# Kernel optimization log

Hardware: AMD Instinct MI355X
Metric: run time of the kernel (lower is better)

## Reference

```python
import jax, jax.numpy as jnp
import numpy as np

N = 100_000   # nodes
E = 1_600_000 # edges (avg degree 16)
IN = 256
OUT = 128
NEG_SLOPE = 0.01  # torch F.leaky_relu default


def setup_inputs() -> dict:
    key = jax.random.key(0)
    k1, k2, k3, k4, k5 = jax.random.split(key, 5)
    h = jax.random.normal(k1, (N, IN), dtype=jnp.float32)
    W = jax.random.normal(k2, (IN, OUT), dtype=jnp.float32) * 0.05  # fc weight (in->out)
    a = jax.random.normal(k3, (2 * OUT,), dtype=jnp.float32) * 0.05  # attn_fc weight, flattened
    src = jax.random.randint(k4, (E,), 0, N, dtype=jnp.int32)
    dst = jax.random.randint(k5, (E,), 0, N, dtype=jnp.int32)
    return {"h": h, "W": W, "a": a, "src": src, "dst": dst, "counter": 3}


def reference(h, W, a, src, dst, counter):
    out_dim = W.shape[1]
    z = h @ W                               # [N, OUT] = fc(h)
    # edge_attention: e = leaky_relu(attn_fc(cat(z[src], z[dst])))
    s = z @ a[:out_dim]                     # [N] src contribution
    t = z @ a[out_dim:]                     # [N] dst contribution
    e = jax.nn.leaky_relu(s[src] + t[dst], NEG_SLOPE)  # [E]
    # segment softmax over incoming edges of each dst node (fixed across iterations)
    m = jax.ops.segment_max(e, dst, num_segments=N)    # [N]
    w = jnp.exp(e - m[dst])                             # [E]
    denom = jax.ops.segment_sum(w, dst, num_segments=N)  # [N]
    alpha = w / denom[dst]                               # [E]
    # nodes with no in-edges keep their previous h (DGL update_all semantics)
    deg = jax.ops.segment_sum(jnp.ones_like(e), dst, num_segments=N)
    has_in = (deg > 0)[:, None]                          # [N,1]
    hcur = z
    for _ in range(int(counter)):
        agg = jax.ops.segment_sum(alpha[:, None] * hcur[src], dst, num_segments=N)  # [N,OUT]
        hcur = jnp.where(has_in, agg, hcur)
    return hcur
```

## Files before the change

### kernel.cpp

```cpp
#include <hip/hip_runtime.h>
#include <math.h>

#define IN_DIM 256
#define OUT_DIM 128
#define BK 1024
#define NBMAX 128

typedef _Float16 f16;
typedef _Float16 f16x2 __attribute__((ext_vector_type(2)));
typedef _Float16 f16x4 __attribute__((ext_vector_type(4)));
typedef _Float16 f16x8 __attribute__((ext_vector_type(8)));
typedef float    f32x4 __attribute__((ext_vector_type(4)));

static inline size_t align256(size_t x){ return (x + 255) & ~size_t(255); }

__global__ void init_kernel(int* __restrict__ gcount, int NB){
  int i = threadIdx.x;
  if (i < NB) gcount[i] = 0;
}

__global__ __launch_bounds__(256) void wprep_kernel(const float* __restrict__ Wm,
    f16* __restrict__ WThi, f16* __restrict__ WTlo){
  int idx = blockIdx.x*256 + threadIdx.x;
  int k = idx >> 7, n = idx & 127;
  float v = Wm[(size_t)k*OUT_DIM + n];
  f16 hi = (f16)v;
  WThi[(size_t)n*IN_DIM + k] = hi;
  WTlo[(size_t)n*IN_DIM + k] = (f16)(v - (float)hi);
}

__global__ __launch_bounds__(256) void gemm_kernel(const float* __restrict__ h,
    const f16* __restrict__ WThi, const f16* __restrict__ WTlo,
    const float* __restrict__ attn_a,
    float* __restrict__ z, f16* __restrict__ zh,
    float* __restrict__ s_arr, float* __restrict__ t_arr, int N){
  __shared__ f16 Ahi[128][40];
  __shared__ f16 Alo[128][40];
  __shared__ f16 Bhi[128][40];
  __shared__ f16 Blo[128][40];

  const int t = threadIdx.x;
  const int l = t & 63;
  const int w = t >> 6;
  const int g = l >> 4;
  const int m15 = l & 15;
  const int row0 = blockIdx.x * 128;

  float as[8], at[8];
  #pragma unroll
  for (int ct=0; ct<8; ct++){
    as[ct] = attn_a[ct*16 + m15];
    at[ct] = attn_a[OUT_DIM + ct*16 + m15];
  }

  f32x4 acc[2][8];
  #pragma unroll
  for (int i=0;i<2;i++)
    #pragma unroll
    for (int j=0;j<8;j++) acc[i][j] = (f32x4){0.f,0.f,0.f,0.f};

  const int ar = t >> 1;
  const int ahalf = (t & 1) << 4;
  for (int k0 = 0; k0 < IN_DIM; k0 += 32){
    {
      int grow = row0 + ar;
      #pragma unroll
      for (int i=0;i<4;i++){
        float4 v = make_float4(0.f,0.f,0.f,0.f);
        if (grow < N) v = *(const float4*)&h[(size_t)grow*IN_DIM + k0 + ahalf + i*4];
        f16 h0=(f16)v.x, h1=(f16)v.y, h2=(f16)v.z, h3=(f16)v.w;
        f16x4 vh = {h0,h1,h2,h3};
        f16x4 vl = {(f16)(v.x-(float)h0),(f16)(v.y-(float)h1),
                    (f16)(v.z-(float)h2),(f16)(v.w-(float)h3)};
        *(f16x4*)&Ahi[ar][ahalf + i*4] = vh;
        *(f16x4*)&Alo[ar][ahalf + i*4] = vl;
      }
      #pragma unroll
      for (int j=0;j<2;j++){
        *(f16x8*)&Bhi[ar][ahalf + j*8] = *(const f16x8*)&WThi[(size_t)ar*IN_DIM + k0 + ahalf + j*8];
        *(f16x8*)&Blo[ar][ahalf + j*8] = *(const f16x8*)&WTlo[(size_t)ar*IN_DIM + k0 + ahalf + j*8];
      }
    }
    __syncthreads();
    f16x8 ah0 = *(const f16x8*)&Ahi[w*32      + m15][g*8];
    f16x8 ah1 = *(const f16x8*)&Ahi[w*32 + 16 + m15][g*8];
    f16x8 al0 = *(const f16x8*)&Alo[w*32      + m15][g*8];
    f16x8 al1 = *(const f16x8*)&Alo[w*32 + 16 + m15][g*8];
    #pragma unroll
    for (int ct=0; ct<8; ct++){
      f16x8 bh = *(const f16x8*)&Bhi[ct*16 + m15][g*8];
      f16x8 bl = *(const f16x8*)&Blo[ct*16 + m15][g*8];
      acc[0][ct] = __builtin_amdgcn_mfma_f32_16x16x32_f16(ah0, bh, acc[0][ct], 0, 0, 0);
      acc[0][ct] = __builtin_amdgcn_mfma_f32_16x16x32_f16(ah0, bl, acc[0][ct], 0, 0, 0);
      acc[0][ct] = __builtin_amdgcn_mfma_f32_16x16x32_f16(al0, bh, acc[0][ct], 0, 0, 0);
      acc[1][ct] = __builtin_amdgcn_mfma_f32_16x16x32_f16(ah1, bh, acc[1][ct], 0, 0, 0);
      acc[1][ct] = __builtin_amdgcn_mfma_f32_16x16x32_f16(ah1, bl, acc[1][ct], 0, 0, 0);
      acc[1][ct] = __builtin_amdgcn_mfma_f32_16x16x32_f16(al1, bh, acc[1][ct], 0, 0, 0);
    }
    __syncthreads();
  }

  #pragma unroll
  for (int rt=0; rt<2; rt++){
    #pragma unroll
    for (int r=0; r<4; r++){
      int grow = row0 + w*32 + rt*16 + g*4 + r;
      float sp = 0.f, tp = 0.f;
      #pragma unroll
      for (int ct=0; ct<8; ct++){
        float v = acc[rt][ct][r];
        if (grow < N){
          z [(size_t)grow*OUT_DIM + ct*16 + m15] = v;
          zh[(size_t)grow*OUT_DIM + ct*16 + m15] = (f16)v;
        }
        sp = fmaf(v, as[ct], sp);
        tp = fmaf(v, at[ct], tp);
      }
      #pragma unroll
      for (int o=1; o<16; o<<=1){ sp += __shfl_xor(sp,o); tp += __shfl_xor(tp,o); }
      if (m15 == 0 && grow < N){ s_arr[grow] = sp; t_arr[grow] = tp; }
    }
  }
}

__global__ __launch_bounds__(256) void count_kernel(const int* __restrict__ dst,
    int* __restrict__ gcount, int E, int NB){
  __shared__ int lh[NBMAX];
  for (int i=threadIdx.x; i<NB; i+=256) lh[i]=0;
  __syncthreads();
  int i = blockIdx.x*blockDim.x + threadIdx.x;
  int stride = gridDim.x*blockDim.x;
  for (; i<E; i+=stride) atomicAdd(&lh[dst[i]>>10], 1);
  __syncthreads();
  for (int i=threadIdx.x; i<NB; i+=256){
    int c = lh[i];
    if (c) atomicAdd(&gcount[i], c);
  }
}

__global__ __launch_bounds__(128) void scanb_kernel(const int* __restrict__ gcount,
    int* __restrict__ gbase, int* __restrict__ gcursor, int* __restrict__ offs,
    int NB, int N, int E){
  int tid = threadIdx.x;
  int v = (tid < NB) ? gcount[tid] : 0;
  int lane = tid & 63, wv = tid >> 6;
  int x = v;
  #pragma unroll
  for (int o=1;o<64;o<<=1){ int y = __shfl_up(x,o); if (lane>=o) x += y; }
  __shared__ int wt[2];
  if (lane==63) wt[wv] = x;
  __syncthreads();
  int off = wv ? wt[0] : 0;
  int excl = off + x - v;
  if (tid < NB){ gbase[tid] = excl; gcursor[tid] = excl; }
  if (tid == 0){ gbase[NB] = E; offs[N] = E; }
}

__global__ __launch_bounds__(256) void scatter_kernel(const int* __restrict__ src,
    const int* __restrict__ dst, const float* __restrict__ s_arr,
    const float* __restrict__ t_arr, int* __restrict__ gcursor,
    int* __restrict__ p_sd, float* __restrict__ p_w, int E, int NB){
  __shared__ int lh[NBMAX];
  __shared__ int lbase[NBMAX];
  for (int i=threadIdx.x;i<NB;i+=256) lh[i]=0;
  __syncthreads();
  int base = blockIdx.x * (256*8);
  int sN[8], dN[8], rk[8];
  float wv[8];
  #pragma unroll
  for (int k=0;k<8;k++){
    int j = base + threadIdx.x + k*256;
    if (j < E){
      int s_ = src[j], d_ = dst[j];
      float e = s_arr[s_] + t_arr[d_];
      e = e > 0.f ? e : 0.01f*e;
      wv[k] = __expf(e);
      sN[k] = s_; dN[k] = d_;
      rk[k] = atomicAdd(&lh[d_>>10], 1);
    } else rk[k] = -1;
  }
  __syncthreads();
  for (int i=threadIdx.x;i<NB;i+=256){
    int c = lh[i];
    lbase[i] = c ? atomicAdd(&gcursor[i], c) : 0;
  }
  __syncthreads();
  #pragma unroll
  for (int k=0;k<8;k++){
    if (rk[k] >= 0){
      int b = dN[k] >> 10;
      int pos = lbase[b] + rk[k];
      p_sd[pos] = sN[k] | ((dN[k] & 1023) << 20);
      p_w[pos]  = wv[k];
    }
  }
}

__global__ __launch_bounds__(512) void bucket_kernel(const int* __restrict__ gbase,
    const int* __restrict__ p_sd, const float* __restrict__ p_w,
    int* __restrict__ offs, int* __restrict__ csr_src, float* __restrict__ csr_alpha,
    int N){
  __shared__ int   hist[BK];
  __shared__ float wsum[BK];
  __shared__ int   loff[BK];
  __shared__ int   wtot[8];
  int b = blockIdx.x;
  int tid = threadIdx.x;
  int e0 = gbase[b], e1 = gbase[b+1];
  int n0 = b << 10;
  int nn = min(BK, N - n0);
  for (int i=tid;i<BK;i+=512){ hist[i]=0; wsum[i]=0.f; }
  __syncthreads();
  for (int j=e0+tid; j<e1; j+=512){
    int dl = p_sd[j] >> 20;
    atomicAdd(&hist[dl], 1);
    atomicAdd(&wsum[dl], p_w[j]);
  }
  __syncthreads();
  int v0 = hist[tid*2], v1 = hist[tid*2+1];
  int tsum = v0 + v1;
  int lane = tid & 63, wv = tid >> 6;
  int x = tsum;
  #pragma unroll
  for (int o=1;o<64;o<<=1){ int y = __shfl_up(x,o); if (lane>=o) x += y; }
  if (lane==63) wtot[wv] = x;
  __syncthreads();
  int woff = 0;
  for (int i=0;i<wv;i++) woff += wtot[i];
  int excl = woff + x - tsum;
  if (tid*2   < nn) offs[n0 + tid*2  ] = e0 + excl;
  loff[tid*2] = excl; excl += v0;
  if (tid*2+1 < nn) offs[n0 + tid*2+1] = e0 + excl;
  loff[tid*2+1] = excl;
  __syncthreads();
  for (int j=e0+tid; j<e1; j+=512){
    int sd = p_sd[j];
    int dl = sd >> 20;
    int r = atomicAdd(&loff[dl], 1);
    csr_src[e0 + r]   = sd & 0xFFFFF;
    csr_alpha[e0 + r] = p_w[j] / wsum[dl];
  }
}

__global__ __launch_bounds__(256) void agg_kernel(const f16* __restrict__ hIn,
    f16* __restrict__ hOut, const float* __restrict__ z, float* __restrict__ out,
    const int* __restrict__ offs, const int* __restrict__ csr_src,
    const float* __restrict__ csr_alpha, const int* __restrict__ counter,
    int it, int N){
  int wv   = threadIdx.x >> 6;
  int lane = threadIdx.x & 63;
  int n = blockIdx.x*4 + wv;
  if (n >= N) return;
  int cntr = counter[0];
  if (cntr <= 0){
    if (it == 0)
      *(float2*)&out[(size_t)n*OUT_DIM + lane*2] =
        *(const float2*)&z[(size_t)n*OUT_DIM + lane*2];
    return;
  }
  if (it >= cntr) return;
  const bool fin = (it == cntr - 1);
  int s0 = offs[n], s1 = offs[n+1];
  if (s0 == s1){
    if (fin)
      *(float2*)&out[(size_t)n*OUT_DIM + lane*2] =
        *(const float2*)&z[(size_t)n*OUT_DIM + lane*2];
    else
      *(f16x2*)&hOut[(size_t)n*OUT_DIM + lane*2] =
        *(const f16x2*)&hIn[(size_t)n*OUT_DIM + lane*2];
    return;
  }
  float2 a0c = {0.f,0.f}, a1c = {0.f,0.f}, a2c = {0.f,0.f}, a3c = {0.f,0.f};
  for (int base = s0; base < s1; base += 64){
    int j = base + lane;
    int   msrc = 0; float malpha = 0.f;
    if (j < s1){ msrc = csr_src[j]; malpha = csr_alpha[j]; }
    int cnt = min(64, s1 - base);
    int k = 0;
    for (; k+4 <= cnt; k += 4){
      int   sk0 = __shfl(msrc, k+0); float w0 = __shfl(malpha, k+0);
      int   sk1 = __shfl(msrc, k+1); float w1 = __shfl(malpha, k+1);
      int   sk2 = __shfl(msrc, k+2); float w2 = __shfl(malpha, k+2);
      int   sk3 = __shfl(msrc, k+3); float w3 = __shfl(malpha, k+3);
      f16x2 v0 = *(const f16x2*)&hIn[(size_t)sk0*OUT_DIM + lane*2];
      f16x2 v1 = *(const f16x2*)&hIn[(size_t)sk1*OUT_DIM + lane*2];
      f16x2 v2 = *(const f16x2*)&hIn[(size_t)sk2*OUT_DIM + lane*2];
      f16x2 v3 = *(const f16x2*)&hIn[(size_t)sk3*OUT_DIM + lane*2];
      a0c.x = fmaf(w0, (float)v0.x, a0c.x); a0c.y = fmaf(w0, (float)v0.y, a0c.y);
      a1c.x = fmaf(w1, (float)v1.x, a1c.x); a1c.y = fmaf(w1, (float)v1.y, a1c.y);
      a2c.x = fmaf(w2, (float)v2.x, a2c.x); a2c.y = fmaf(w2, (float)v2.y, a2c.y);
      a3c.x = fmaf(w3, (float)v3.x, a3c.x); a3c.y = fmaf(w3, (float)v3.y, a3c.y);
    }
    for (; k < cnt; k++){
      int   sk = __shfl(msrc, k); float wk = __shfl(malpha, k);
      f16x2 v = *(const f16x2*)&hIn[(size_t)sk*OUT_DIM + lane*2];
      a0c.x = fmaf(wk, (float)v.x, a0c.x); a0c.y = fmaf(wk, (float)v.y, a0c.y);
    }
  }
  float2 res;
  res.x = (a0c.x + a1c.x) + (a2c.x + a3c.x);
  res.y = (a0c.y + a1c.y) + (a2c.y + a3c.y);
  if (fin){
    *(float2*)&out[(size_t)n*OUT_DIM + lane*2] = res;
  } else {
    f16x2 o = {(f16)res.x, (f16)res.y};
    *(f16x2*)&hOut[(size_t)n*OUT_DIM + lane*2] = o;
  }
}

extern "C" void kernel_launch(void* const* d_in, const int* in_sizes, int n_in,
                              void* d_out, int out_size, void* d_ws, size_t ws_size,
                              hipStream_t stream){
  const float* h   = (const float*)d_in[0];
  const float* Wm  = (const float*)d_in[1];
  const float* a   = (const float*)d_in[2];
  const int*   src = (const int*)d_in[3];
  const int*   dst = (const int*)d_in[4];
  const int* counter = (const int*)d_in[5];
  const int N = in_sizes[0] / IN_DIM;
  const int E = in_sizes[3];
  const int NB = (N + BK - 1) / BK;
  float* out = (float*)d_out;

  char* p = (char*)d_ws;
  auto alloc = [&](size_t bytes){ void* r = (void*)p; p += align256(bytes); return r; };
  float* z         = (float*)alloc((size_t)N*OUT_DIM*4);
  f16*   hA        = (f16*)  alloc((size_t)N*OUT_DIM*2);
  f16*   hB        = (f16*)  alloc((size_t)N*OUT_DIM*2);
  float* s_arr     = (float*)alloc((size_t)N*4);
  float* t_arr     = (float*)alloc((size_t)N*4);
  int*   p_sd      = (int*)  alloc((size_t)E*4);
  float* p_w       = (float*)alloc((size_t)E*4);
  int*   csr_src   = (int*)  alloc((size_t)E*4);
  float* csr_alpha = (float*)alloc((size_t)E*4);
  int*   offs      = (int*)  alloc((size_t)(N+1)*4);
  int*   gcount    = (int*)  alloc((size_t)NBMAX*4);
  int*   gbase     = (int*)  alloc((size_t)(NBMAX+1)*4);
  int*   gcursor   = (int*)  alloc((size_t)NBMAX*4);
  f16*   WThi      = (f16*)  alloc((size_t)IN_DIM*OUT_DIM*2);
  f16*   WTlo      = (f16*)  alloc((size_t)IN_DIM*OUT_DIM*2);

  init_kernel<<<1, 128, 0, stream>>>(gcount, NB);
  wprep_kernel<<<(IN_DIM*OUT_DIM)/256, 256, 0, stream>>>(Wm, WThi, WTlo);
  gemm_kernel<<<(N+127)/128, 256, 0, stream>>>(h, WThi, WTlo, a, z, hA, s_arr, t_arr, N);
  count_kernel<<<512, 256, 0, stream>>>(dst, gcount, E, NB);
  scanb_kernel<<<1, 128, 0, stream>>>(gcount, gbase, gcursor, offs, NB, N, E);
  scatter_kernel<<<(E + 2047)/2048, 256, 0, stream>>>(src, dst, s_arr, t_arr,
                                                      gcursor, p_sd, p_w, E, NB);
  bucket_kernel<<<NB, 512, 0, stream>>>(gbase, p_sd, p_w, offs, csr_src, csr_alpha, N);
  agg_kernel<<<(N+3)/4, 256, 0, stream>>>(hA, hB, z, out, offs, csr_src, csr_alpha, counter, 0, N);
  agg_kernel<<<(N+3)/4, 256, 0, stream>>>(hB, hA, z, out, offs, csr_src, csr_alpha, counter, 1, N);
  agg_kernel<<<(N+3)/4, 256, 0, stream>>>(hA, hB, z, out, offs, csr_src, csr_alpha, counter, 2, N);
}
```

Measured before the change: 372.2 us.

## Load GEMM operands directly to registers and pack CSR src/alpha pairs

The GEMM kernel drops its LDS staging and barriers. Each wave now loads its h rows and W columns straight from global memory into MFMA operand registers, using a 2x2 wave tiling of 64x64 per wave. The s/t attention partials are combined across the two column-waves through a small shared buffer. Separately, the CSR source index and alpha are interleaved into one int2 array, so the aggregation kernel issues a single 8-byte load per edge instead of two loads, at the cost of redundant global/L2 reads of W and h without LDS reuse.

```diff
diff --git a/kernel.cpp b/kernel.cpp
--- a/kernel.cpp
+++ b/kernel.cpp
@@ -8,7 +8,6 @@
 
 typedef _Float16 f16;
 typedef _Float16 f16x2 __attribute__((ext_vector_type(2)));
-typedef _Float16 f16x4 __attribute__((ext_vector_type(4)));
 typedef _Float16 f16x8 __attribute__((ext_vector_type(8)));
 typedef float    f32x4 __attribute__((ext_vector_type(4)));
 
@@ -34,91 +33,105 @@
     const float* __restrict__ attn_a,
     float* __restrict__ z, f16* __restrict__ zh,
     float* __restrict__ s_arr, float* __restrict__ t_arr, int N){
-  __shared__ f16 Ahi[128][40];
-  __shared__ f16 Alo[128][40];
-  __shared__ f16 Bhi[128][40];
-  __shared__ f16 Blo[128][40];
+  __shared__ float spart[128][2];
+  __shared__ float tpart[128][2];
 
   const int t = threadIdx.x;
   const int l = t & 63;
   const int w = t >> 6;
-  const int g = l >> 4;
+  const int wr = w >> 1;
+  const int wc = w & 1;
   const int m15 = l & 15;
+  const int g   = l >> 4;
   const int row0 = blockIdx.x * 128;
 
-  float as[8], at[8];
-  #pragma unroll
-  for (int ct=0; ct<8; ct++){
-    as[ct] = attn_a[ct*16 + m15];
-    at[ct] = attn_a[OUT_DIM + ct*16 + m15];
-  }
-
-  f32x4 acc[2][8];
-  #pragma unroll
-  for (int i=0;i<2;i++)
+  const float* hrow[4];
+  #pragma unroll
+  for (int rt=0; rt<4; rt++){
+    int r = row0 + wr*64 + rt*16 + m15;
+    if (r > N-1) r = N-1;
+    hrow[rt] = h + (size_t)r*IN_DIM;
+  }
+  const f16* bhp[4]; const f16* blp[4];
+  #pragma unroll
+  for (int ct=0; ct<4; ct++){
+    int n = wc*64 + ct*16 + m15;
+    bhp[ct] = WThi + (size_t)n*IN_DIM;
+    blp[ct] = WTlo + (size_t)n*IN_DIM;
+  }
+
+  f32x4 acc[4][4];
+  #pragma unroll
+  for (int i=0;i<4;i++)
     #pragma unroll
-    for (int j=0;j<8;j++) acc[i][j] = (f32x4){0.f,0.f,0.f,0.f};
-
-  const int ar = t >> 1;
-  const int ahalf = (t & 1) << 4;
+    for (int j=0;j<4;j++) acc[i][j] = (f32x4){0.f,0.f,0.f,0.f};
+
+  const int g8 = g*8;
+  #pragma unroll 2
   for (int k0 = 0; k0 < IN_DIM; k0 += 32){
-    {
-      int grow = row0 + ar;
+    f16x8 ah[4], al[4];
+    #pragma unroll
+    for (int rt=0;rt<4;rt++){
+      float4 v0 = *(const float4*)&hrow[rt][k0+g8];
+      float4 v1 = *(const float4*)&hrow[rt][k0+g8+4];
+      float vv[8] = {v0.x,v0.y,v0.z,v0.w,v1.x,v1.y,v1.z,v1.w};
+      f16x8 hh, ll;
       #pragma unroll
-      for (int i=0;i<4;i++){
-        float4 v = make_float4(0.f,0.f,0.f,0.f);
-        if (grow < N) v = *(const float4*)&h[(size_t)grow*IN_DIM + k0 + ahalf + i*4];
-        f16 h0=(f16)v.x, h1=(f16)v.y, h2=(f16)v.z, h3=(f16)v.w;
-        f16x4 vh = {h0,h1,h2,h3};
-        f16x4 vl = {(f16)(v.x-(float)h0),(f16)(v.y-(float)h1),
-                    (f16)(v.z-(float)h2),(f16)(v.w-(float)h3)};
-        *(f16x4*)&Ahi[ar][ahalf + i*4] = vh;
-        *(f16x4*)&Alo[ar][ahalf + i*4] = vl;
+      for (int q=0;q<8;q++){
+        f16 hq = (f16)vv[q];
+        hh[q] = hq;
+        ll[q] = (f16)(vv[q] - (float)hq);
       }
+      ah[rt] = hh; al[rt] = ll;
+    }
+    #pragma unroll
+    for (int ct=0;ct<4;ct++){
+      f16x8 bh = *(const f16x8*)&bhp[ct][k0+g8];
+      f16x8 bl = *(const f16x8*)&blp[ct][k0+g8];
       #pragma unroll
-      for (int j=0;j<2;j++){
-        *(f16x8*)&Bhi[ar][ahalf + j*8] = *(const f16x8*)&WThi[(size_t)ar*IN_DIM + k0 + ahalf + j*8];
-        *(f16x8*)&Blo[ar][ahalf + j*8] = *(const f16x8*)&WTlo[(size_t)ar*IN_DIM + k0 + ahalf + j*8];
+      for (int rt=0;rt<4;rt++){
+        acc[rt][ct] = __builtin_amdgcn_mfma_f32_16x16x32_f16(ah[rt], bh, acc[rt][ct], 0, 0, 0);
+        acc[rt][ct] = __builtin_amdgcn_mfma_f32_16x16x32_f16(ah[rt], bl, acc[rt][ct], 0, 0, 0);
+        acc[rt][ct] = __builtin_amdgcn_mfma_f32_16x16x32_f16(al[rt], bh, acc[rt][ct], 0, 0, 0);
       }
     }
-    __syncthreads();
-    f16x8 ah0 = *(const f16x8*)&Ahi[w*32      + m15][g*8];
-    f16x8 ah1 = *(const f16x8*)&Ahi[w*32 + 16 + m15][g*8];
-    f16x8 al0 = *(const f16x8*)&Alo[w*32      + m15][g*8];
-    f16x8 al1 = *(const f16x8*)&Alo[w*32 + 16 + m15][g*8];
-    #pragma unroll
-    for (int ct=0; ct<8; ct++){
-      f16x8 bh = *(const f16x8*)&Bhi[ct*16 + m15][g*8];
-      f16x8 bl = *(const f16x8*)&Blo[ct*16 + m15][g*8];
-      acc[0][ct] = __builtin_amdgcn_mfma_f32_16x16x32_f16(ah0, bh, acc[0][ct], 0, 0, 0);
-      acc[0][ct] = __builtin_amdgcn_mfma_f32_16x16x32_f16(ah0, bl, acc[0][ct], 0, 0, 0);
-      acc[0][ct] = __builtin_amdgcn_mfma_f32_16x16x32_f16(al0, bh, acc[0][ct], 0, 0, 0);
-      acc[1][ct] = __builtin_amdgcn_mfma_f32_16x16x32_f16(ah1, bh, acc[1][ct], 0, 0, 0);
-      acc[1][ct] = __builtin_amdgcn_mfma_f32_16x16x32_f16(ah1, bl, acc[1][ct], 0, 0, 0);
-      acc[1][ct] = __builtin_amdgcn_mfma_f32_16x16x32_f16(al1, bh, acc[1][ct], 0, 0, 0);
-    }
-    __syncthreads();
-  }
-
-  #pragma unroll
-  for (int rt=0; rt<2; rt++){
+  }
+
+  float as_[4], at_[4];
+  #pragma unroll
+  for (int ct=0; ct<4; ct++){
+    as_[ct] = attn_a[wc*64 + ct*16 + m15];
+    at_[ct] = attn_a[OUT_DIM + wc*64 + ct*16 + m15];
+  }
+
+  #pragma unroll
+  for (int rt=0; rt<4; rt++){
     #pragma unroll
     for (int r=0; r<4; r++){
-      int grow = row0 + w*32 + rt*16 + g*4 + r;
+      int lrow = wr*64 + rt*16 + g*4 + r;
+      int grow = row0 + lrow;
       float sp = 0.f, tp = 0.f;
       #pragma unroll
-      for (int ct=0; ct<8; ct++){
+      for (int ct=0; ct<4; ct++){
         float v = acc[rt][ct][r];
         if (grow < N){
-          z [(size_t)grow*OUT_DIM + ct*16 + m15] = v;
-          zh[(size_t)grow*OUT_DIM + ct*16 + m15] = (f16)v;
+          z [(size_t)grow*OUT_DIM + wc*64 + ct*16 + m15] = v;
+          zh[(size_t)grow*OUT_DIM + wc*64 + ct*16 + m15] = (f16)v;
         }
-        sp = fmaf(v, as[ct], sp);
-        tp = fmaf(v, at[ct], tp);
+        sp = fmaf(v, as_[ct], sp);
+        tp = fmaf(v, at_[ct], tp);
       }
       #pragma unroll
       for (int o=1; o<16; o<<=1){ sp += __shfl_xor(sp,o); tp += __shfl_xor(tp,o); }
-      if (m15 == 0 && grow < N){ s_arr[grow] = sp; t_arr[grow] = tp; }
+      if (m15 == 0){ spart[lrow][wc] = sp; tpart[lrow][wc] = tp; }
+    }
+  }
+  __syncthreads();
+  if (t < 128){
+    int grow = row0 + t;
+    if (grow < N){
+      s_arr[grow] = spart[t][0] + spart[t][1];
+      t_arr[grow] = tpart[t][0] + tpart[t][1];
     }
   }
 }
@@ -198,8 +211,7 @@
 
 __global__ __launch_bounds__(512) void bucket_kernel(const int* __restrict__ gbase,
     const int* __restrict__ p_sd, const float* __restrict__ p_w,
-    int* __restrict__ offs, int* __restrict__ csr_src, float* __restrict__ csr_alpha,
-    int N){
+    int* __restrict__ offs, int2* __restrict__ csrp, int N){
   __shared__ int   hist[BK];
   __shared__ float wsum[BK];
   __shared__ int   loff[BK];
@@ -237,16 +249,15 @@
     int sd = p_sd[j];
     int dl = sd >> 20;
     int r = atomicAdd(&loff[dl], 1);
-    csr_src[e0 + r]   = sd & 0xFFFFF;
-    csr_alpha[e0 + r] = p_w[j] / wsum[dl];
+    int2 pk; pk.x = sd & 0xFFFFF; pk.y = __float_as_int(p_w[j] / wsum[dl]);
+    csrp[e0 + r] = pk;
   }
 }
 
 __global__ __launch_bounds__(256) void agg_kernel(const f16* __restrict__ hIn,
     f16* __restrict__ hOut, const float* __restrict__ z, float* __restrict__ out,
-    const int* __restrict__ offs, const int* __restrict__ csr_src,
-    const float* __restrict__ csr_alpha, const int* __restrict__ counter,
-    int it, int N){
+    const int* __restrict__ offs, const int2* __restrict__ csrp,
+    const int* __restrict__ counter, int it, int N){
   int wv   = threadIdx.x >> 6;
   int lane = threadIdx.x & 63;
   int n = blockIdx.x*4 + wv;
@@ -273,15 +284,15 @@
   float2 a0c = {0.f,0.f}, a1c = {0.f,0.f}, a2c = {0.f,0.f}, a3c = {0.f,0.f};
   for (int base = s0; base < s1; base += 64){
     int j = base + lane;
-    int   msrc = 0; float malpha = 0.f;
-    if (j < s1){ msrc = csr_src[j]; malpha = csr_alpha[j]; }
+    int2 me = make_int2(0, 0);
+    if (j < s1) me = csrp[j];
     int cnt = min(64, s1 - base);
     int k = 0;
     for (; k+4 <= cnt; k += 4){
-      int   sk0 = __shfl(msrc, k+0); float w0 = __shfl(malpha, k+0);
-      int   sk1 = __shfl(msrc, k+1); float w1 = __shfl(malpha, k+1);
-      int   sk2 = __shfl(msrc, k+2); float w2 = __shfl(malpha, k+2);
-      int   sk3 = __shfl(msrc, k+3); float w3 = __shfl(malpha, k+3);
+      int sk0 = __shfl(me.x, k+0); float w0 = __int_as_float(__shfl(me.y, k+0));
+      int sk1 = __shfl(me.x, k+1); float w1 = __int_as_float(__shfl(me.y, k+1));
+      int sk2 = __shfl(me.x, k+2); float w2 = __int_as_float(__shfl(me.y, k+2));
+      int sk3 = __shfl(me.x, k+3); float w3 = __int_as_float(__shfl(me.y, k+3));
       f16x2 v0 = *(const f16x2*)&hIn[(size_t)sk0*OUT_DIM + lane*2];
       f16x2 v1 = *(const f16x2*)&hIn[(size_t)sk1*OUT_DIM + lane*2];
       f16x2 v2 = *(const f16x2*)&hIn[(size_t)sk2*OUT_DIM + lane*2];
@@ -292,7 +303,7 @@
       a3c.x = fmaf(w3, (float)v3.x, a3c.x); a3c.y = fmaf(w3, (float)v3.y, a3c.y);
     }
     for (; k < cnt; k++){
-      int   sk = __shfl(msrc, k); float wk = __shfl(malpha, k);
+      int sk = __shfl(me.x, k); float wk = __int_as_float(__shfl(me.y, k));
       f16x2 v = *(const f16x2*)&hIn[(size_t)sk*OUT_DIM + lane*2];
       a0c.x = fmaf(wk, (float)v.x, a0c.x); a0c.y = fmaf(wk, (float)v.y, a0c.y);
     }
@@ -331,8 +342,7 @@
   float* t_arr     = (float*)alloc((size_t)N*4);
   int*   p_sd      = (int*)  alloc((size_t)E*4);
   float* p_w       = (float*)alloc((size_t)E*4);
-  int*   csr_src   = (int*)  alloc((size_t)E*4);
-  float* csr_alpha = (float*)alloc((size_t)E*4);
+  int2*  csrp      = (int2*) alloc((size_t)E*8);
   int*   offs      = (int*)  alloc((size_t)(N+1)*4);
   int*   gcount    = (int*)  alloc((size_t)NBMAX*4);
   int*   gbase     = (int*)  alloc((size_t)(NBMAX+1)*4);
@@ -347,8 +357,8 @@
   scanb_kernel<<<1, 128, 0, stream>>>(gcount, gbase, gcursor, offs, NB, N, E);
   scatter_kernel<<<(E + 2047)/2048, 256, 0, stream>>>(src, dst, s_arr, t_arr,
                                                       gcursor, p_sd, p_w, E, NB);
-  bucket_kernel<<<NB, 512, 0, stream>>>(gbase, p_sd, p_w, offs, csr_src, csr_alpha, N);
-  agg_kernel<<<(N+3)/4, 256, 0, stream>>>(hA, hB, z, out, offs, csr_src, csr_alpha, counter, 0, N);
-  agg_kernel<<<(N+3)/4, 256, 0, stream>>>(hB, hA, z, out, offs, csr_src, csr_alpha, counter, 1, N);
-  agg_kernel<<<(N+3)/4, 256, 0, stream>>>(hA, hB, z, out, offs, csr_src, csr_alpha, counter, 2, N);
-}
+  bucket_kernel<<<NB, 512, 0, stream>>>(gbase, p_sd, p_w, offs, csrp, N);
+  agg_kernel<<<(N+3)/4, 256, 0, stream>>>(hA, hB, z, out, offs, csrp, counter, 0, N);
+  agg_kernel<<<(N+3)/4, 256, 0, stream>>>(hB, hA, z, out, offs, csrp, counter, 1, N);
+  agg_kernel<<<(N+3)/4, 256, 0, stream>>>(hA, hB, z, out, offs, csrp, counter, 2, N);
+}
```

After: 383.0 us. 1.03x slower.
